# Optimization experiments

Measured on AMD Instinct MI355X. Metric: run time of the kernel, lower is better.

The kernel has to match this reference:

```python
import jax, jax.numpy as jnp
import numpy as np

D_MODEL = 1024
N_HEADS = 16
D_K = D_MODEL // N_HEADS
LN_EPS = 1e-5


def setup_inputs() -> dict:
    key = jax.random.key(0)
    ks = jax.random.split(key, 12)
    B, S, D = 4, 2048, D_MODEL
    s = 1.0 / np.sqrt(D)
    return {
        "Q": jax.random.normal(ks[0], (B, S, D), jnp.float32),
        "K": jax.random.normal(ks[1], (B, S, D), jnp.float32),
        "V": jax.random.normal(ks[2], (B, S, D), jnp.float32),
        "W_q": jax.random.normal(ks[3], (D, D), jnp.float32) * s,
        "b_q": jnp.zeros((D,), jnp.float32),
        "W_k": jax.random.normal(ks[4], (D, D), jnp.float32) * s,
        "b_k": jnp.zeros((D,), jnp.float32),
        "W_v": jax.random.normal(ks[5], (D, D), jnp.float32) * s,
        "b_v": jnp.zeros((D,), jnp.float32),
        "W_o": jax.random.normal(ks[6], (D, D), jnp.float32) * s,
        "b_o": jnp.zeros((D,), jnp.float32),
        "ln_gamma": jnp.ones((D,), jnp.float32),
        "ln_beta": jnp.zeros((D,), jnp.float32),
    }


def _split_heads(x):  # (B,S,D) -> (B,H,S,Dk)
    B, S, _ = x.shape
    return x.reshape(B, S, N_HEADS, D_K).transpose(0, 2, 1, 3)


def reference(Q, K, V, W_q, b_q, W_k, b_k, W_v, b_v, W_o, b_o, ln_gamma, ln_beta):
    # Linear projections (torch Linear: x @ W^T + b)
    q = Q @ W_q.T + b_q  # (B,S,D) -- also the residual in this module
    k = K @ W_k.T + b_k
    v = V @ W_v.T + b_v
    qh, kh, vh = _split_heads(q), _split_heads(k), _split_heads(v)
    scale = 1.0 / jnp.sqrt(jnp.float32(D_K))
    scores = jnp.einsum("bhqd,bhkd->bhqk", qh, kh) * scale
    attn = jax.nn.softmax(scores, axis=-1)  # dropout = identity (eval)
    ctx = jnp.einsum("bhqk,bhkd->bhqd", attn, vh)
    B, H, S, Dk = ctx.shape
    ctx = ctx.transpose(0, 2, 1, 3).reshape(B, S, H * Dk)  # (B,S,D)
    out = ctx @ W_o.T + b_o
    # residual uses projected Q (module quirk), then LayerNorm
    x = out + q
    mu = jnp.mean(x, axis=-1, keepdims=True)
    var = jnp.mean((x - mu) ** 2, axis=-1, keepdims=True)
    return (x - mu) * jax.lax.rsqrt(var + LN_EPS) * ln_gamma + ln_beta
```

## Files before the change

### kernel.cpp

```cpp
#include <hip/hip_runtime.h>
#include <hip/hip_bf16.h>
#include <stdint.h>

#define D_MODEL 1024
#define NH 16
#define DKH 64
#define NBATCH 4
#define SEQ 2048
#define NROWS (NBATCH*SEQ)

typedef __bf16 bf16;
typedef __bf16 bf16x8 __attribute__((ext_vector_type(8)));
typedef __bf16 bf16x4 __attribute__((ext_vector_type(4)));
typedef float f32x4 __attribute__((ext_vector_type(4)));

static __device__ __forceinline__ f32x4 fzero4() {
  f32x4 z; z[0] = 0.f; z[1] = 0.f; z[2] = 0.f; z[3] = 0.f; return z;
}

static __device__ __forceinline__ float fast_exp2(float x) {
  return __builtin_amdgcn_exp2f(x);
}

static __device__ __forceinline__ void gload16(const bf16* g, bf16* lds) {
  __builtin_amdgcn_global_load_lds(
      (const __attribute__((address_space(1))) uint32_t*)(uintptr_t)g,
      (__attribute__((address_space(3))) uint32_t*)(uintptr_t)lds,
      16, 0, 0);
}

__global__ __launch_bounds__(256) void cvt_w4(const float* __restrict__ a,
                                              const float* __restrict__ b,
                                              const float* __restrict__ c,
                                              const float* __restrict__ d,
                                              bf16* __restrict__ out) {
  const float* srcs[4] = {a, b, c, d};
  const float* s = srcs[blockIdx.y];
  int i = blockIdx.x * 256 + threadIdx.x;
  float4 v = ((const float4*)s)[i];
  bf16x4 o;
  o[0] = (bf16)v.x; o[1] = (bf16)v.y; o[2] = (bf16)v.z; o[3] = (bf16)v.w;
  ((bf16x4*)out)[blockIdx.y * (D_MODEL * D_MODEL / 4) + i] = o;
}

__global__ __launch_bounds__(256) void gemm_qkv(const float* __restrict__ Qin,
                                                const float* __restrict__ Kin,
                                                const float* __restrict__ Vin,
                                                const bf16* __restrict__ Wall,
                                                const float* __restrict__ bq,
                                                const float* __restrict__ bk,
                                                const float* __restrict__ bv,
                                                bf16* __restrict__ qbf,
                                                bf16* __restrict__ kpb,
                                                bf16* __restrict__ vtb) {
  __shared__ __align__(16) bf16 As[2][128 * 64];
  __shared__ __align__(16) bf16 Bs[2][128 * 64];
  const int orig = blockIdx.x + ((blockIdx.y + (blockIdx.z << 6)) << 3);
  const int work = ((orig & 7) * 192) + (orig >> 3);
  const int bn = work & 7;
  const int bm = (work >> 3) & 63;
  const int z = work >> 9;

  const float* A = z == 0 ? Qin : (z == 1 ? Kin : Vin);
  const bf16* B = Wall + (size_t)z * D_MODEL * D_MODEL;
  const float* bias = z == 0 ? bq : (z == 1 ? bk : bv);
  const int N = D_MODEL;

  const int t = threadIdx.x, w = t >> 6, l = t & 63;
  const int wm = w >> 1, wn = w & 1;
  const int lr = l & 15, g = l >> 4;
  const int rowA0 = bm * 128, colB0 = bn * 128;

  const int c8 = l & 7;
  const int rbase = l >> 3;

  f32x4 a0[4], a1[4];

#define LOADA(K0)                                                             \
  {                                                                           \
    _Pragma("unroll")                                                         \
    for (int i = 0; i < 4; i++) {                                             \
      int r = (w * 4 + i) * 8 + rbase;                                        \
      const float* p = A + (size_t)(rowA0 + r) * D_MODEL + (K0) + c8 * 8;     \
      a0[i] = *(const f32x4*)p;                                               \
      a1[i] = *(const f32x4*)(p + 4);                                         \
    }                                                                         \
  }
#define WRITEA(BUF)                                                           \
  {                                                                           \
    _Pragma("unroll")                                                         \
    for (int i = 0; i < 4; i++) {                                             \
      int r = (w * 4 + i) * 8 + rbase;                                        \
      bf16x8 o;                                                               \
      _Pragma("unroll")                                                       \
      for (int j = 0; j < 4; j++) { o[j] = (bf16)a0[i][j]; o[4 + j] = (bf16)a1[i][j]; } \
      *(bf16x8*)((char*)As[BUF] + r * 128 + ((c8 * 16) ^ ((r & 7) << 4))) = o; \
    }                                                                         \
  }
#define STAGEB(K0, BUF)                                                       \
  {                                                                           \
    _Pragma("unroll")                                                         \
    for (int i = 0; i < 4; i++) {                                             \
      int r = (w * 4 + i) * 8 + rbase;                                        \
      int cb = (c8 * 16) ^ ((r & 7) << 4);                                    \
      gload16(B + (size_t)(colB0 + r) * D_MODEL + (K0) + (cb >> 1),           \
              &Bs[BUF][(w * 4 + i) * 512]);                                   \
    }                                                                         \
  }

  f32x4 acc[4][4];
#pragma unroll
  for (int m = 0; m < 4; m++)
#pragma unroll
    for (int n = 0; n < 4; n++) acc[m][n] = fzero4();

  LOADA(0); STAGEB(0, 0);
  asm volatile("s_waitcnt vmcnt(0)" ::: "memory");
  WRITEA(0);
  asm volatile("s_waitcnt lgkmcnt(0)" ::: "memory");
  __builtin_amdgcn_s_barrier();
  asm volatile("" ::: "memory");
  LOADA(64); STAGEB(64, 1);

  int cur = 0;
  for (int kt = 0; kt < 16; ++kt) {
#pragma unroll
    for (int kk = 0; kk < 2; kk++) {
      bf16x8 av[4], bv4[4];
#pragma unroll
      for (int m = 0; m < 4; m++) {
        int row = wm * 64 + m * 16 + lr;
        int off = row * 128 + ((kk * 64 + g * 16) ^ ((row & 7) << 4));
        av[m] = *(const bf16x8*)((const char*)As[cur] + off);
      }
#pragma unroll
      for (int n = 0; n < 4; n++) {
        int row = wn * 64 + n * 16 + lr;
        int off = row * 128 + ((kk * 64 + g * 16) ^ ((row & 7) << 4));
        bv4[n] = *(const bf16x8*)((const char*)Bs[cur] + off);
      }
#pragma unroll
      for (int m = 0; m < 4; m++)
#pragma unroll
        for (int n = 0; n < 4; n++)
          acc[m][n] = __builtin_amdgcn_mfma_f32_16x16x32_bf16(av[m], bv4[n], acc[m][n], 0, 0, 0);
    }
    if (kt < 15) {
      asm volatile("s_waitcnt vmcnt(0)" ::: "memory");
      WRITEA(cur ^ 1);
    }
    asm volatile("s_waitcnt lgkmcnt(0)" ::: "memory");
    __builtin_amdgcn_s_barrier();
    asm volatile("" ::: "memory");
    if (kt < 14) { LOADA((kt + 2) * 64); STAGEB((kt + 2) * 64, cur); }
    cur ^= 1;
  }
#undef LOADA
#undef WRITEA
#undef STAGEB

  if (z == 2) {
#pragma unroll
    for (int n = 0; n < 4; n++) {
      int col = colB0 + wn * 64 + n * 16 + lr;
      float bc = bias[col];
      int hh = col >> 6, dh = col & 63;
#pragma unroll
      for (int m = 0; m < 4; m++) {
        int row = rowA0 + wm * 64 + m * 16 + g * 4;
        int bb = row >> 11;
        int ss = row & 2047;
        int pos = (ss & ~31) + g * 8 + (m & 1) * 4;
        bf16x4 o;
#pragma unroll
        for (int j = 0; j < 4; j++) o[j] = (bf16)(acc[m][n][j] + bc);
        *(bf16x4*)(vtb + (((size_t)(bb * NH + hh)) * DKH + dh) * SEQ + pos) = o;
      }
    }
  } else {
    bf16* Cb = z == 0 ? qbf : kpb;
    const float bscale = z == 0 ? 0.180336880111f : 1.0f;
#pragma unroll
    for (int n = 0; n < 4; n++) {
      int col = colB0 + wn * 64 + n * 16 + lr;
      float bc = bias[col];
#pragma unroll
      for (int m = 0; m < 4; m++) {
#pragma unroll
        for (int j = 0; j < 4; j++) {
          int row = rowA0 + wm * 64 + m * 16 + g * 4 + j;
          Cb[(size_t)row * N + col] = (bf16)((acc[m][n][j] + bc) * bscale);
        }
      }
    }
  }
}

#define STAGE_G(K0, BUF)                                                      \
  {                                                                           \
    _Pragma("unroll")                                                         \
    for (int i = 0; i < 4; i++) {                                             \
      int r = (w * 4 + i) * 8 + (l >> 3);                                     \
      int cb = ((l & 7) * 16) ^ ((r & 7) << 4);                               \
      gload16(A + (size_t)(rowA0 + r) * D_MODEL + (K0) + (cb >> 1),           \
              &As[BUF][(w * 4 + i) * 512]);                                   \
      gload16(B + (size_t)(colB0 + r) * D_MODEL + (K0) + (cb >> 1),           \
              &Bs[BUF][(w * 4 + i) * 512]);                                   \
    }                                                                         \
  }

__global__ __launch_bounds__(256) void gemm_o(const bf16* __restrict__ A,
                                              const bf16* __restrict__ B,
                                              const float* __restrict__ bias,
                                              float* __restrict__ Cf) {
  __shared__ __align__(16) bf16 As[2][128 * 64];
  __shared__ __align__(16) bf16 Bs[2][128 * 64];
  const int orig = blockIdx.x + (blockIdx.y << 3);
  const int work = ((orig & 7) * 64) + (orig >> 3);
  const int bn = work & 7, bm = work >> 3;
  const int t = threadIdx.x, w = t >> 6, l = t & 63;
  const int wm = w >> 1, wn = w & 1;
  const int lr = l & 15, g = l >> 4;
  const int rowA0 = bm * 128, colB0 = bn * 128;
  const int N = D_MODEL;

  f32x4 acc[4][4];
#pragma unroll
  for (int m = 0; m < 4; m++)
#pragma unroll
    for (int n = 0; n < 4; n++) acc[m][n] = fzero4();

  STAGE_G(0, 0);
  STAGE_G(64, 1);
  int cur = 0;
  for (int kt = 0; kt < 16; ++kt) {
    if (kt < 15) asm volatile("s_waitcnt vmcnt(8)" ::: "memory");
    else         asm volatile("s_waitcnt vmcnt(0)" ::: "memory");
    __builtin_amdgcn_s_barrier();
    asm volatile("" ::: "memory");
#pragma unroll
    for (int kk = 0; kk < 2; kk++) {
      bf16x8 av[4], bv4[4];
#pragma unroll
      for (int m = 0; m < 4; m++) {
        int row = wm * 64 + m * 16 + lr;
        int off = row * 128 + ((kk * 64 + g * 16) ^ ((row & 7) << 4));
        av[m] = *(const bf16x8*)((const char*)As[cur] + off);
      }
#pragma unroll
      for (int n = 0; n < 4; n++) {
        int row = wn * 64 + n * 16 + lr;
        int off = row * 128 + ((kk * 64 + g * 16) ^ ((row & 7) << 4));
        bv4[n] = *(const bf16x8*)((const char*)Bs[cur] + off);
      }
#pragma unroll
      for (int m = 0; m < 4; m++)
#pragma unroll
        for (int n = 0; n < 4; n++)
          acc[m][n] = __builtin_amdgcn_mfma_f32_16x16x32_bf16(av[m], bv4[n], acc[m][n], 0, 0, 0);
    }
    asm volatile("s_waitcnt lgkmcnt(0)" ::: "memory");
    __builtin_amdgcn_s_barrier();
    if (kt < 14) STAGE_G((kt + 2) * 64, cur);
    cur ^= 1;
  }

#pragma unroll
  for (int n = 0; n < 4; n++) {
    int col = colB0 + wn * 64 + n * 16 + lr;
    float bc = bias[col];
#pragma unroll
    for (int m = 0; m < 4; m++) {
#pragma unroll
      for (int j = 0; j < 4; j++) {
        int row = rowA0 + wm * 64 + m * 16 + g * 4 + j;
        Cf[(size_t)row * N + col] = acc[m][n][j] + bc;
      }
    }
  }
}

__global__ __launch_bounds__(256, 4) void attn_fwd(const bf16* __restrict__ Qp,
                                                   const bf16* __restrict__ Kp,
                                                   const bf16* __restrict__ Vt,
                                                   bf16* __restrict__ Ctx) {
  __shared__ __align__(16) bf16 Ks[2][64 * 64];
  __shared__ __align__(16) bf16 Vs[2][64 * 64];
  const int bid0 = blockIdx.x;
  const int bid = ((bid0 & 7) << 7) | (bid0 >> 3);
  const int qt = bid & 15;
  const int h = (bid >> 4) & 15;
  const int b = bid >> 8;
  const int w = threadIdx.x >> 6, l = threadIdx.x & 63;
  const int lr = l & 15, g = l >> 4;
  const int q0 = qt * 128 + w * 32;

  const size_t qkBase = ((size_t)b * SEQ) * D_MODEL + h * DKH;
  const size_t vtBase = ((size_t)(b * NH + h)) * DKH * SEQ;
  const bf16* Kg = Kp + qkBase;
  const bf16* Vg = Vt + vtBase;

  const int sr = w * 8 + (l >> 3);
  const int scb = (l & 7) * 16;

  bf16x8 qf[2][2];
#pragma unroll
  for (int f = 0; f < 2; f++)
#pragma unroll
    for (int kk = 0; kk < 2; kk++)
      qf[f][kk] = *(const bf16x8*)(Qp + qkBase + (size_t)(q0 + f * 16 + lr) * D_MODEL + kk * 32 + g * 8);

  bf16x8 vone;
#pragma unroll
  for (int j = 0; j < 8; j++) vone[j] = (bf16)1.0f;

  f32x4 ctx[2][5];
#pragma unroll
  for (int f = 0; f < 2; f++)
#pragma unroll
    for (int n = 0; n < 5; n++) ctx[f][n] = fzero4();

#define STAGE(T, BUF)                                                         \
  {                                                                           \
    const int _s0 = (T) * 64;                                                 \
    _Pragma("unroll")                                                         \
    for (int i = 0; i < 2; i++) {                                             \
      int r = i * 32 + sr;                                                    \
      int cb = scb ^ ((r & 7) << 4);                                          \
      gload16(Kg + (size_t)(_s0 + r) * D_MODEL + (cb >> 1),                   \
              &Ks[BUF][i * 2048 + w * 512]);                                  \
      gload16(Vg + (size_t)r * SEQ + _s0 + (cb >> 1),                         \
              &Vs[BUF][i * 2048 + w * 512]);                                  \
    }                                                                         \
  }

  STAGE(0, 0);
  int cur = 0;
  for (int t = 0; t < SEQ / 64; ++t) {
    if (t + 1 < SEQ / 64) {
      STAGE(t + 1, cur ^ 1);
      asm volatile("s_waitcnt vmcnt(4)" ::: "memory");
    } else {
      asm volatile("s_waitcnt vmcnt(0)" ::: "memory");
    }
    __builtin_amdgcn_s_barrier();
    asm volatile("" ::: "memory");

#pragma unroll
    for (int ss = 0; ss < 2; ++ss) {
      bf16x8 ka[2][2];
#pragma unroll
      for (int hf = 0; hf < 2; hf++) {
        int row = ss * 32 + hf * 16 + lr;
#pragma unroll
        for (int kk = 0; kk < 2; kk++) {
          int off = row * 128 + ((kk * 64 + g * 16) ^ ((row & 7) << 4));
          ka[hf][kk] = *(const bf16x8*)((const char*)Ks[cur] + off);
        }
      }
      bf16x8 vb[4];
#pragma unroll
      for (int n = 0; n < 4; n++) {
        int row = n * 16 + lr;
        int off = row * 128 + ((ss * 64 + g * 16) ^ ((row & 7) << 4));
        vb[n] = *(const bf16x8*)((const char*)Vs[cur] + off);
      }

#pragma unroll
      for (int f = 0; f < 2; f++) {
        f32x4 sc[2];
        __builtin_amdgcn_s_setprio(1);
#pragma unroll
        for (int hf = 0; hf < 2; hf++) {
          f32x4 tt = fzero4();
          tt = __builtin_amdgcn_mfma_f32_16x16x32_bf16(ka[hf][0], qf[f][0], tt, 0, 0, 0);
          tt = __builtin_amdgcn_mfma_f32_16x16x32_bf16(ka[hf][1], qf[f][1], tt, 0, 0, 0);
          sc[hf] = tt;
        }
        __builtin_amdgcn_s_setprio(0);
        float p[8];
#pragma unroll
        for (int hf = 0; hf < 2; hf++)
#pragma unroll
          for (int j = 0; j < 4; j++)
            p[hf * 4 + j] = fast_exp2(sc[hf][j]);
        bf16x8 pa;
#pragma unroll
        for (int j = 0; j < 8; j++) pa[j] = (bf16)p[j];
        __builtin_amdgcn_s_setprio(1);
#pragma unroll
        for (int n = 0; n < 4; n++)
          ctx[f][n] = __builtin_amdgcn_mfma_f32_16x16x32_bf16(pa, vb[n], ctx[f][n], 0, 0, 0);
        ctx[f][4] = __builtin_amdgcn_mfma_f32_16x16x32_bf16(pa, vone, ctx[f][4], 0, 0, 0);
        __builtin_amdgcn_s_setprio(0);
      }
    }
    asm volatile("" ::: "memory");
    __builtin_amdgcn_s_barrier();
    cur ^= 1;
  }
#undef STAGE

#pragma unroll
  for (int f = 0; f < 2; f++) {
#pragma unroll
    for (int j = 0; j < 4; j++) {
      float lj = 1.0f / ctx[f][4][j];
      int s = q0 + f * 16 + g * 4 + j;
      size_t base = ((size_t)b * SEQ + s) * D_MODEL + h * DKH;
#pragma unroll
      for (int n = 0; n < 4; n++)
        Ctx[base + n * 16 + lr] = (bf16)(ctx[f][n][j] * lj);
    }
  }
}

__global__ __launch_bounds__(256) void ln_res(const float* __restrict__ O,
                                              const bf16* __restrict__ Rb,
                                              const float* __restrict__ gam,
                                              const float* __restrict__ bet,
                                              float* __restrict__ out) {
  const int row = blockIdx.x, t = threadIdx.x;
  const size_t idx = (size_t)row * 256 + t;
  const float4 o = ((const float4*)O)[idx];
  const bf16x4 rb = ((const bf16x4*)Rb)[idx];
  const float rs = 5.545177444479562f;
  float x0 = o.x + (float)rb[0] * rs, x1 = o.y + (float)rb[1] * rs;
  float x2 = o.z + (float)rb[2] * rs, x3 = o.w + (float)rb[3] * rs;
  float s = x0 + x1 + x2 + x3;
  float q = x0 * x0 + x1 * x1 + x2 * x2 + x3 * x3;
#pragma unroll
  for (int off = 32; off >= 1; off >>= 1) {
    s += __shfl_xor(s, off);
    q += __shfl_xor(q, off);
  }
  __shared__ float red[8];
  const int wid = t >> 6;
  if ((t & 63) == 0) { red[wid] = s; red[4 + wid] = q; }
  __syncthreads();
  s = red[0] + red[1] + red[2] + red[3];
  q = red[4] + red[5] + red[6] + red[7];
  const float mu = s * (1.f / 1024.f);
  const float rinv = rsqrtf(q * (1.f / 1024.f) - mu * mu + 1e-5f);
  const float4 g4 = ((const float4*)gam)[t];
  const float4 b4 = ((const float4*)bet)[t];
  float4 y;
  y.x = (x0 - mu) * rinv * g4.x + b4.x;
  y.y = (x1 - mu) * rinv * g4.y + b4.y;
  y.z = (x2 - mu) * rinv * g4.z + b4.z;
  y.w = (x3 - mu) * rinv * g4.w + b4.w;
  ((float4*)out)[idx] = y;
}

extern "C" void kernel_launch(void* const* d_in, const int* in_sizes, int n_in,
                              void* d_out, int out_size, void* d_ws, size_t ws_size,
                              hipStream_t stream) {
  const float* Q   = (const float*)d_in[0];
  const float* Kx  = (const float*)d_in[1];
  const float* V   = (const float*)d_in[2];
  const float* Wq  = (const float*)d_in[3];
  const float* bq  = (const float*)d_in[4];
  const float* Wk  = (const float*)d_in[5];
  const float* bk  = (const float*)d_in[6];
  const float* Wv  = (const float*)d_in[7];
  const float* bv  = (const float*)d_in[8];
  const float* Wo  = (const float*)d_in[9];
  const float* bo  = (const float*)d_in[10];
  const float* gam = (const float*)d_in[11];
  const float* bet = (const float*)d_in[12];
  float* out = (float*)d_out;

  char* ws = (char*)d_ws;
  const size_t MB = 1ull << 20;
  bf16* wall = (bf16*)(ws);
  bf16* qbf  = (bf16*)(ws + 8 * MB);
  bf16* kpb  = (bf16*)(ws + 24 * MB);
  bf16* vtb  = (bf16*)(ws + 40 * MB);
  bf16* ctx  = (bf16*)(ws + 56 * MB);
  float* attnout = (float*)(ws + 72 * MB);

  const int nW4 = D_MODEL * D_MODEL / 4;
  dim3 cb(256);

  cvt_w4<<<dim3(nW4 / 256, 4), cb, 0, stream>>>(Wq, Wk, Wv, Wo, wall);

  gemm_qkv<<<dim3(8, 64, 3), cb, 0, stream>>>(Q, Kx, V, wall, bq, bk, bv, qbf, kpb, vtb);

  attn_fwd<<<NBATCH * NH * 16, cb, 0, stream>>>(qbf, kpb, vtb, ctx);

  gemm_o<<<dim3(8, 64), cb, 0, stream>>>(ctx, wall + 3ull * D_MODEL * D_MODEL, bo, attnout);
  ln_res<<<NROWS, cb, 0, stream>>>(attnout, qbf, gam, bet, out);
}
```

Baseline: 194.6 us.

## Double-buffer A-tile registers to deepen QKV projection GEMM prefetch pipeline

Splits the fp32 A-tile prefetch registers into even/odd sets and unrolls the K loop by two so global loads for tile k+2 and k+3 are issued while computing earlier tiles. Uses partial vmcnt waits instead of full drains so the B-tile direct-to-LDS loads can stay in flight. This aims to hide global memory latency in the QKV projection kernel, at the cost of more VGPRs, which may reduce occupancy.

After: 186.9 us. -3.9%, faster.

```diff
diff --git a/kernel.cpp b/kernel.cpp
--- a/kernel.cpp
+++ b/kernel.cpp
@@ -74,26 +74,27 @@
   const int c8 = l & 7;
   const int rbase = l >> 3;
 
-  f32x4 a0[4], a1[4];
-
-#define LOADA(K0)                                                             \
+  f32x4 aE0[4], aE1[4];
+  f32x4 aO0[4], aO1[4];
+
+#define LOADA(K0, R0, R1)                                                     \
   {                                                                           \
     _Pragma("unroll")                                                         \
     for (int i = 0; i < 4; i++) {                                             \
       int r = (w * 4 + i) * 8 + rbase;                                        \
       const float* p = A + (size_t)(rowA0 + r) * D_MODEL + (K0) + c8 * 8;     \
-      a0[i] = *(const f32x4*)p;                                               \
-      a1[i] = *(const f32x4*)(p + 4);                                         \
+      R0[i] = *(const f32x4*)p;                                               \
+      R1[i] = *(const f32x4*)(p + 4);                                         \
     }                                                                         \
   }
-#define WRITEA(BUF)                                                           \
+#define WRITEA(BUF, R0, R1)                                                   \
   {                                                                           \
     _Pragma("unroll")                                                         \
     for (int i = 0; i < 4; i++) {                                             \
       int r = (w * 4 + i) * 8 + rbase;                                        \
       bf16x8 o;                                                               \
       _Pragma("unroll")                                                       \
-      for (int j = 0; j < 4; j++) { o[j] = (bf16)a0[i][j]; o[4 + j] = (bf16)a1[i][j]; } \
+      for (int j = 0; j < 4; j++) { o[j] = (bf16)R0[i][j]; o[4 + j] = (bf16)R1[i][j]; } \
       *(bf16x8*)((char*)As[BUF] + r * 128 + ((c8 * 16) ^ ((r & 7) << 4))) = o; \
     }                                                                         \
   }
@@ -107,6 +108,30 @@
               &Bs[BUF][(w * 4 + i) * 512]);                                   \
     }                                                                         \
   }
+#define COMPUTE(BUF)                                                          \
+  {                                                                           \
+    _Pragma("unroll")                                                         \
+    for (int kk = 0; kk < 2; kk++) {                                          \
+      bf16x8 av[4], bv4[4];                                                   \
+      _Pragma("unroll")                                                       \
+      for (int m = 0; m < 4; m++) {                                           \
+        int row = wm * 64 + m * 16 + lr;                                      \
+        int off = row * 128 + ((kk * 64 + g * 16) ^ ((row & 7) << 4));        \
+        av[m] = *(const bf16x8*)((const char*)As[BUF] + off);                 \
+      }                                                                       \
+      _Pragma("unroll")                                                       \
+      for (int n = 0; n < 4; n++) {                                           \
+        int row = wn * 64 + n * 16 + lr;                                      \
+        int off = row * 128 + ((kk * 64 + g * 16) ^ ((row & 7) << 4));        \
+        bv4[n] = *(const bf16x8*)((const char*)Bs[BUF] + off);                \
+      }                                                                       \
+      _Pragma("unroll")                                                       \
+      for (int m = 0; m < 4; m++)                                             \
+        _Pragma("unroll")                                                     \
+        for (int n = 0; n < 4; n++)                                           \
+          acc[m][n] = __builtin_amdgcn_mfma_f32_16x16x32_bf16(av[m], bv4[n], acc[m][n], 0, 0, 0); \
+    }                                                                         \
+  }
 
   f32x4 acc[4][4];
 #pragma unroll
@@ -114,50 +139,42 @@
 #pragma unroll
     for (int n = 0; n < 4; n++) acc[m][n] = fzero4();
 
-  LOADA(0); STAGEB(0, 0);
-  asm volatile("s_waitcnt vmcnt(0)" ::: "memory");
-  WRITEA(0);
+  LOADA(0, aE0, aE1); STAGEB(0, 0);
+  LOADA(64, aO0, aO1); STAGEB(64, 1);
+  asm volatile("s_waitcnt vmcnt(12)" ::: "memory");
+  WRITEA(0, aE0, aE1);
   asm volatile("s_waitcnt lgkmcnt(0)" ::: "memory");
   __builtin_amdgcn_s_barrier();
   asm volatile("" ::: "memory");
-  LOADA(64); STAGEB(64, 1);
-
-  int cur = 0;
-  for (int kt = 0; kt < 16; ++kt) {
-#pragma unroll
-    for (int kk = 0; kk < 2; kk++) {
-      bf16x8 av[4], bv4[4];
-#pragma unroll
-      for (int m = 0; m < 4; m++) {
-        int row = wm * 64 + m * 16 + lr;
-        int off = row * 128 + ((kk * 64 + g * 16) ^ ((row & 7) << 4));
-        av[m] = *(const bf16x8*)((const char*)As[cur] + off);
-      }
-#pragma unroll
-      for (int n = 0; n < 4; n++) {
-        int row = wn * 64 + n * 16 + lr;
-        int off = row * 128 + ((kk * 64 + g * 16) ^ ((row & 7) << 4));
-        bv4[n] = *(const bf16x8*)((const char*)Bs[cur] + off);
-      }
-#pragma unroll
-      for (int m = 0; m < 4; m++)
-#pragma unroll
-        for (int n = 0; n < 4; n++)
-          acc[m][n] = __builtin_amdgcn_mfma_f32_16x16x32_bf16(av[m], bv4[n], acc[m][n], 0, 0, 0);
-    }
-    if (kt < 15) {
-      asm volatile("s_waitcnt vmcnt(0)" ::: "memory");
-      WRITEA(cur ^ 1);
-    }
+
+  for (int it = 0; it < 8; ++it) {
+    const int kt0 = 2 * it;
+    if (it < 7) LOADA((kt0 + 2) * 64, aE0, aE1);
+    COMPUTE(0);
+    if (it < 7) asm volatile("s_waitcnt vmcnt(8)" ::: "memory");
+    else        asm volatile("s_waitcnt vmcnt(0)" ::: "memory");
+    WRITEA(1, aO0, aO1);
     asm volatile("s_waitcnt lgkmcnt(0)" ::: "memory");
     __builtin_amdgcn_s_barrier();
     asm volatile("" ::: "memory");
-    if (kt < 14) { LOADA((kt + 2) * 64); STAGEB((kt + 2) * 64, cur); }
-    cur ^= 1;
+    if (it < 7) STAGEB((kt0 + 2) * 64, 0);
+    if (it < 7) {
+      LOADA((kt0 + 3) * 64, aO0, aO1);
+      COMPUTE(1);
+      asm volatile("s_waitcnt vmcnt(8)" ::: "memory");
+      WRITEA(0, aE0, aE1);
+      asm volatile("s_waitcnt lgkmcnt(0)" ::: "memory");
+      __builtin_amdgcn_s_barrier();
+      asm volatile("" ::: "memory");
+      STAGEB((kt0 + 3) * 64, 1);
+    } else {
+      COMPUTE(1);
+    }
   }
 #undef LOADA
 #undef WRITEA
 #undef STAGEB
+#undef COMPUTE
 
   if (z == 2) {
 #pragma unroll
```
